# Kernel optimization log

Hardware: AMD Instinct MI355X
Metric: run time of the kernel (lower is better)

The kernel has to match this reference:

```python
import jax, jax.numpy as jnp
import numpy as np

N = 8192   # number of points (p) == number of reference points (r); must match for final bmm
D = 1024   # feature width of the Linear projections


def setup_inputs() -> dict:
    key = jax.random.key(0)
    ks = jax.random.split(key, 8)
    s = 1.0 / np.sqrt(D)
    return {
        "p": jax.random.normal(ks[0], (N, D), dtype=jnp.float32),
        "r": jax.random.normal(ks[1], (N, D), dtype=jnp.float32),
        "Wh": jax.random.uniform(ks[2], (D, D), jnp.float32, -s, s),
        "bh": jax.random.uniform(ks[3], (D,), jnp.float32, -s, s),
        "Wl": jax.random.uniform(ks[4], (D, D), jnp.float32, -s, s),
        "bl": jax.random.uniform(ks[5], (D,), jnp.float32, -s, s),
        "Wg": jax.random.uniform(ks[6], (D, D), jnp.float32, -s, s),
        "bg": jax.random.uniform(ks[7], (D,), jnp.float32, -s, s),
    }


def reference(p, r, Wh, bh, Wl, bl, Wg, bg):
    # Linear projections (torch Linear: x @ W.T + b)
    q = p @ Wh.T + bh          # [N, D]  M_h(p)
    k = r @ Wl.T + bl          # [N, D]  M_l(r)
    v = p @ Wg.T + bg          # [N, D]  M_g(p)
    scores = q @ k.T           # [N, N]  == bmm(q[None], k[None].transpose(1,2))[0]
    # torch softmax dim=1 on [1, N, N] normalizes over the QUERY axis -> axis=0 here
    attn = jax.nn.softmax(scores, axis=0)
    return p + attn @ v        # residual add
```

## Files before the change

kernel.cpp:

```cpp
#include <hip/hip_runtime.h>
#include <hip/hip_fp16.h>

typedef _Float16 f16;
typedef __attribute__((ext_vector_type(8))) _Float16 f16x8;
typedef __attribute__((ext_vector_type(4))) float f32x4;

#define NPTS 8192
#define DIM  1024
#define HL2E 0.721347520444482f
#define S2SHIFT 50.0f

__device__ __forceinline__ void glds16(const void* g, void* l) {
  __builtin_amdgcn_global_load_lds(
      (const __attribute__((address_space(1))) void*)g,
      (__attribute__((address_space(3))) void*)l, 16, 0, 0);
}

__global__ void cvt_f32_f16(const float* __restrict__ src, f16* __restrict__ dst, int n) {
  int i = (blockIdx.x * 256 + threadIdx.x) * 8;
  if (i >= n) return;
  const float4* s = (const float4*)(src + i);
  float4 a = s[0], b = s[1];
  f16x8 o;
  o[0] = (f16)a.x; o[1] = (f16)a.y; o[2] = (f16)a.z; o[3] = (f16)a.w;
  o[4] = (f16)b.x; o[5] = (f16)b.y; o[6] = (f16)b.z; o[7] = (f16)b.w;
  *(f16x8*)(dst + i) = o;
}

__global__ void zero_f32(float* __restrict__ p, int n) {
  int i = blockIdx.x * 256 + threadIdx.x;
  if (i < n) p[i] = 0.f;
}

__global__ void mk_scales(const float* __restrict__ colsum,
                          f16* __restrict__ ics2, f16* __restrict__ ics4) {
  int j = blockIdx.x * 256 + threadIdx.x;
  float r2 = rsqrtf(colsum[j]);
  ics2[j] = (f16)r2;
  ics4[j] = (f16)sqrtf(r2);
}

__global__ void vscale(f16* __restrict__ vt, const f16* __restrict__ ics2) {
  long i = ((long)blockIdx.x * 256 + threadIdx.x) * 8;
  f16x8 v = *(f16x8*)(vt + i);
  f16x8 s = *(const f16x8*)(ics2 + (i & (NPTS - 1)));
  *(f16x8*)(vt + i) = v * s;
}

template<int EPI, int SWZ>
__global__ __launch_bounds__(256, 2)
void gemm_bt(const f16* __restrict__ A, int lda,
             const f16* __restrict__ B, int ldb,
             int M, int N, int K,
             const float* __restrict__ bias,
             void* __restrict__ Cout, int ldc,
             const float* __restrict__ Res, int ldr,
             float* __restrict__ colsum, const f16* __restrict__ ics4) {
  __shared__ f16 sA[128 * 32];
  __shared__ f16 sB[128 * 32];
  const int t = threadIdx.x;
  const int w = t >> 6, l = t & 63;
  const int wm = (w >> 1) * 64, wn = (w & 1) * 64;
  long bi, bj;
  if (SWZ) {
    bi = (long)(blockIdx.x & 63) * 128;
    bj = (long)(blockIdx.x >> 6) * 128;
  } else {
    bi = (long)blockIdx.y * 128;
    bj = (long)blockIdx.x * 128;
  }
  const int lr = l & 15, lk = (l >> 4) * 8;

  const int grow = w * 16 + (l >> 2);
  const int gcol = (l & 3) * 8;
  const f16* gA = A + (bi + grow) * (long)lda + gcol;
  const f16* gB = B + (bj + grow) * (long)ldb + gcol;
  f16* lA0 = sA + (w * 16) * 32;
  f16* lA1 = sA + (64 + w * 16) * 32;
  f16* lB0 = sB + (w * 16) * 32;
  f16* lB1 = sB + (64 + w * 16) * 32;

  const int sr = t >> 2, sc = (t & 3) * 8;
  const f16* gAs = A + (bi + sr) * (long)lda + sc;
  f16x8 ra0 = {}, ra1 = {}, icv = {};
  if (EPI == 3) {
    ra0 = *(const f16x8*)gAs;
    ra1 = *(const f16x8*)(gAs + 64l * lda);
    icv = *(const f16x8*)(ics4 + sc);
  }

  f32x4 acc[4][4] = {};

  for (int k0 = 0; k0 < K; k0 += 32) {
    __syncthreads();
    if (EPI == 3) {
      f16x8 t0 = ra0 * icv; t0 = t0 * t0;
      f16x8 t1 = ra1 * icv; t1 = t1 * t1;
      *(f16x8*)(sA + sr * 32 + sc) = t0;
      *(f16x8*)(sA + (sr + 64) * 32 + sc) = t1;
    } else {
      glds16(gA, lA0);
      glds16(gA + 64l * lda, lA1);
      gA += 32;
    }
    glds16(gB, lB0);
    glds16(gB + 64l * ldb, lB1);
    gB += 32;
    __syncthreads();
    if (EPI == 3 && k0 + 32 < K) {
      gAs += 32;
      ra0 = *(const f16x8*)gAs;
      ra1 = *(const f16x8*)(gAs + 64l * lda);
      icv = *(const f16x8*)(ics4 + k0 + 32 + sc);
    }
    f16x8 af[4], bf[4];
#pragma unroll
    for (int mt = 0; mt < 4; mt++)
      af[mt] = *(const f16x8*)(sA + (wm + mt * 16 + lr) * 32 + lk);
#pragma unroll
    for (int nt = 0; nt < 4; nt++)
      bf[nt] = *(const f16x8*)(sB + (wn + nt * 16 + lr) * 32 + lk);
#pragma unroll
    for (int mt = 0; mt < 4; mt++)
#pragma unroll
      for (int nt = 0; nt < 4; nt++)
        acc[mt][nt] = __builtin_amdgcn_mfma_f32_16x16x32_f16(af[mt], bf[nt], acc[mt][nt], 0, 0, 0);
  }

  const int rbase = (l >> 4) * 4;
#pragma unroll
  for (int nt = 0; nt < 4; nt++) {
    const long col = bj + wn + nt * 16 + lr;
    float csum = 0.f;
#pragma unroll
    for (int mt = 0; mt < 4; mt++) {
      const long row0 = bi + wm + mt * 16 + rbase;
      if (EPI == 0) {
        float bb = bias[col];
        f16* C = (f16*)Cout;
#pragma unroll
        for (int g = 0; g < 4; g++)
          C[(row0 + g) * ldc + col] = (f16)(acc[mt][nt][g] + bb);
      } else if (EPI == 1) {
        float bb = bias[col];
        union { unsigned long long u; f16 h[4]; } pk;
#pragma unroll
        for (int g = 0; g < 4; g++) pk.h[g] = (f16)(acc[mt][nt][g] + bb);
        *(unsigned long long*)((f16*)Cout + col * (long)ldc + row0) = pk.u;
      } else if (EPI == 3) {
        float* C = (float*)Cout;
#pragma unroll
        for (int g = 0; g < 4; g++)
          C[(row0 + g) * ldc + col] = acc[mt][nt][g] + Res[(row0 + g) * (long)ldr + col];
      } else {
        f16* C = (f16*)Cout;
#pragma unroll
        for (int g = 0; g < 4; g++) {
          float e = exp2f((acc[mt][nt][g] - S2SHIFT) * HL2E);
          e = fminf(e, 240.f);
          f16 eh = (f16)e;
          C[(row0 + g) * ldc + col] = eh;
          float ef = (float)eh;
          csum += ef * ef;
        }
      }
    }
    if (EPI == 4) {
      csum += __shfl_xor(csum, 16);
      csum += __shfl_xor(csum, 32);
      if (l < 16) atomicAdd(colsum + col, csum);
    }
  }
}

extern "C" void kernel_launch(void* const* d_in, const int* in_sizes, int n_in,
                              void* d_out, int out_size, void* d_ws, size_t ws_size,
                              hipStream_t stream) {
  const float* p  = (const float*)d_in[0];
  const float* r  = (const float*)d_in[1];
  const float* Wh = (const float*)d_in[2];
  const float* bh = (const float*)d_in[3];
  const float* Wl = (const float*)d_in[4];
  const float* bl = (const float*)d_in[5];
  const float* Wg = (const float*)d_in[6];
  const float* bg = (const float*)d_in[7];
  float* out = (float*)d_out;

  char* ws = (char*)d_ws;
  f16* q_h  = (f16*)(ws + (0ull  << 20));
  f16* k_h  = (f16*)(ws + (16ull << 20));
  f16* vt_h = (f16*)(ws + (32ull << 20));
  f16* p_h  = (f16*)(ws + (48ull << 20));
  f16* r_h  = (f16*)(ws + (64ull << 20));
  f16* wh_h = (f16*)(ws + (80ull << 20));
  f16* wl_h = (f16*)(ws + (82ull << 20));
  f16* wg_h = (f16*)(ws + (84ull << 20));
  f16* S    = (f16*)(ws + (96ull << 20));
  float* colsum = (float*)(ws + (224ull << 20));
  f16* ics2 = (f16*)(ws + (225ull << 20));
  f16* ics4 = (f16*)(ws + (226ull << 20));

  const int nP = NPTS * DIM, nW = DIM * DIM;
  cvt_f32_f16<<<nP / 2048, 256, 0, stream>>>(p,  p_h,  nP);
  cvt_f32_f16<<<nP / 2048, 256, 0, stream>>>(r,  r_h,  nP);
  cvt_f32_f16<<<nW / 2048, 256, 0, stream>>>(Wh, wh_h, nW);
  cvt_f32_f16<<<nW / 2048, 256, 0, stream>>>(Wl, wl_h, nW);
  cvt_f32_f16<<<nW / 2048, 256, 0, stream>>>(Wg, wg_h, nW);
  zero_f32<<<NPTS / 256, 256, 0, stream>>>(colsum, NPTS);

  dim3 blk(256);
  gemm_bt<0, 1><<<512, blk, 0, stream>>>(
      p_h, DIM, wh_h, DIM, NPTS, DIM, DIM, bh, q_h, DIM, nullptr, 0, nullptr, nullptr);
  gemm_bt<0, 1><<<512, blk, 0, stream>>>(
      r_h, DIM, wl_h, DIM, NPTS, DIM, DIM, bl, k_h, DIM, nullptr, 0, nullptr, nullptr);
  gemm_bt<1, 1><<<512, blk, 0, stream>>>(
      p_h, DIM, wg_h, DIM, NPTS, DIM, DIM, bg, vt_h, NPTS, nullptr, 0, nullptr, nullptr);
  gemm_bt<4, 0><<<dim3(NPTS / 128, NPTS / 128), blk, 0, stream>>>(
      q_h, DIM, k_h, DIM, NPTS, NPTS, DIM, nullptr, S, NPTS, nullptr, 0, colsum, nullptr);
  mk_scales<<<NPTS / 256, 256, 0, stream>>>(colsum, ics2, ics4);
  vscale<<<(NPTS / 8) * (DIM / 256), 256, 0, stream>>>(vt_h, ics2);
  gemm_bt<3, 1><<<512, blk, 0, stream>>>(
      S, NPTS, vt_h, NPTS, NPTS, DIM, NPTS, nullptr, out, DIM, p, DIM, colsum, ics4);
}
```

Measured before the change: 584.8 us.

## Double-buffer LDS tiles in the GEMM main loop with one barrier per step

The shared A and B tiles are doubled so the global-to-LDS loads for the next K-slice are issued into the spare buffer while the MFMA work runs on the current one. A prologue fills the first buffer, and the loop now has a single __syncthreads per iteration instead of two. The EPI==3 path, which scales A in registers, gets the same prefetch-then-store treatment into the alternate buffer. LDS use per block doubles to 32KB, which could limit occupancy, and the overlap depends on the compiler not waiting on the outstanding loads before the compute.

```diff
diff --git a/kernel.cpp b/kernel.cpp
--- a/kernel.cpp
+++ b/kernel.cpp
@@ -9,6 +9,7 @@
 #define DIM  1024
 #define HL2E 0.721347520444482f
 #define S2SHIFT 50.0f
+#define TBUF (128 * 32)
 
 __device__ __forceinline__ void glds16(const void* g, void* l) {
   __builtin_amdgcn_global_load_lds(
@@ -56,8 +57,8 @@
              void* __restrict__ Cout, int ldc,
              const float* __restrict__ Res, int ldr,
              float* __restrict__ colsum, const f16* __restrict__ ics4) {
-  __shared__ f16 sA[128 * 32];
-  __shared__ f16 sB[128 * 32];
+  __shared__ f16 sA[2 * TBUF];
+  __shared__ f16 sB[2 * TBUF];
   const int t = threadIdx.x;
   const int w = t >> 6, l = t & 63;
   const int wm = (w >> 1) * 64, wn = (w & 1) * 64;
@@ -75,51 +76,71 @@
   const int gcol = (l & 3) * 8;
   const f16* gA = A + (bi + grow) * (long)lda + gcol;
   const f16* gB = B + (bj + grow) * (long)ldb + gcol;
-  f16* lA0 = sA + (w * 16) * 32;
-  f16* lA1 = sA + (64 + w * 16) * 32;
-  f16* lB0 = sB + (w * 16) * 32;
-  f16* lB1 = sB + (64 + w * 16) * 32;
+  const int lw0 = (w * 16) * 32;
+  const int lw1 = (64 + w * 16) * 32;
 
   const int sr = t >> 2, sc = (t & 3) * 8;
   const f16* gAs = A + (bi + sr) * (long)lda + sc;
   f16x8 ra0 = {}, ra1 = {}, icv = {};
+
+  const int nk = K >> 5;
+
   if (EPI == 3) {
     ra0 = *(const f16x8*)gAs;
     ra1 = *(const f16x8*)(gAs + 64l * lda);
     icv = *(const f16x8*)(ics4 + sc);
-  }
-
-  f32x4 acc[4][4] = {};
-
-  for (int k0 = 0; k0 < K; k0 += 32) {
-    __syncthreads();
-    if (EPI == 3) {
-      f16x8 t0 = ra0 * icv; t0 = t0 * t0;
-      f16x8 t1 = ra1 * icv; t1 = t1 * t1;
-      *(f16x8*)(sA + sr * 32 + sc) = t0;
-      *(f16x8*)(sA + (sr + 64) * 32 + sc) = t1;
-    } else {
-      glds16(gA, lA0);
-      glds16(gA + 64l * lda, lA1);
-      gA += 32;
-    }
-    glds16(gB, lB0);
-    glds16(gB + 64l * ldb, lB1);
-    gB += 32;
-    __syncthreads();
-    if (EPI == 3 && k0 + 32 < K) {
+    f16x8 t0 = ra0 * icv; t0 = t0 * t0;
+    f16x8 t1 = ra1 * icv; t1 = t1 * t1;
+    *(f16x8*)(sA + sr * 32 + sc) = t0;
+    *(f16x8*)(sA + (sr + 64) * 32 + sc) = t1;
+    if (nk > 1) {
       gAs += 32;
       ra0 = *(const f16x8*)gAs;
       ra1 = *(const f16x8*)(gAs + 64l * lda);
-      icv = *(const f16x8*)(ics4 + k0 + 32 + sc);
+      icv = *(const f16x8*)(ics4 + 32 + sc);
+    }
+  } else {
+    glds16(gA, sA + lw0);
+    glds16(gA + 64l * lda, sA + lw1);
+    gA += 32;
+  }
+  glds16(gB, sB + lw0);
+  glds16(gB + 64l * ldb, sB + lw1);
+  gB += 32;
+
+  f32x4 acc[4][4] = {};
+
+  for (int k = 0; k < nk; k++) {
+    const int cur = (k & 1) * TBUF, nxt = TBUF - cur;
+    __syncthreads();
+    if (k + 1 < nk) {
+      if (EPI == 3) {
+        f16x8 t0 = ra0 * icv; t0 = t0 * t0;
+        f16x8 t1 = ra1 * icv; t1 = t1 * t1;
+        *(f16x8*)(sA + nxt + sr * 32 + sc) = t0;
+        *(f16x8*)(sA + nxt + (sr + 64) * 32 + sc) = t1;
+        if (k + 2 < nk) {
+          gAs += 32;
+          ra0 = *(const f16x8*)gAs;
+          ra1 = *(const f16x8*)(gAs + 64l * lda);
+          icv = *(const f16x8*)(ics4 + (k + 2) * 32 + sc);
+        }
+      } else {
+        glds16(gA, sA + nxt + lw0);
+        glds16(gA + 64l * lda, sA + nxt + lw1);
+        gA += 32;
+      }
+      glds16(gB, sB + nxt + lw0);
+      glds16(gB + 64l * ldb, sB + nxt + lw1);
+      gB += 32;
     }
     f16x8 af[4], bf[4];
 #pragma unroll
     for (int mt = 0; mt < 4; mt++)
-      af[mt] = *(const f16x8*)(sA + (wm + mt * 16 + lr) * 32 + lk);
+      af[mt] = *(const f16x8*)(sA + cur + (wm + mt * 16 + lr) * 32 + lk);
 #pragma unroll
     for (int nt = 0; nt < 4; nt++)
-      bf[nt] = *(const f16x8*)(sB + (wn + nt * 16 + lr) * 32 + lk);
+      bf[nt] = *(const f16x8*)(sB + cur + (wn + nt * 16 + lr) * 32 + lk);
 #pragma unroll
     for (int mt = 0; mt < 4; mt++)
 #pragma unroll
```

Result: no change. 581.5 us (-0.6%).
